# Kernel optimization log

Measured on AMD Instinct MI355X. Metric: run time of the kernel, lower is better.

Reference implementation:

```python
import jax, jax.numpy as jnp
import numpy as np
from jax import lax

B, N, C_IN, C_OUT = 4, 8192, 64, 128
STRIDE, RADIUS, K, L = 4, 0.1, 32, 2
EPS = 1e-5
M = N // STRIDE


def _bn(x, g, b):
    # training-mode batch norm, channel-first layout (B, C, ...)
    axes = (0,) + tuple(range(2, x.ndim))
    mean = jnp.mean(x, axis=axes, keepdims=True)
    var = jnp.mean((x - mean) ** 2, axis=axes, keepdims=True)
    sh = (1, -1) + (1,) * (x.ndim - 2)
    return (x - mean) * lax.rsqrt(var + EPS) * g.reshape(sh) + b.reshape(sh)


def _fps(points, m):
    # farthest point sampling starting at index 0 (matches fps_cuda semantics)
    b, n, _ = points.shape
    bi = jnp.arange(b)

    def body(carry, _):
        dis, last = carry
        lp = points[bi, last]  # (b,3)
        d = jnp.sum((points - lp[:, None, :]) ** 2, -1)
        dis = jnp.minimum(dis, d)
        return (dis, jnp.argmax(dis, -1).astype(jnp.int32)), last

    init = (jnp.full((b, n), 1e10, points.dtype), jnp.zeros((b,), jnp.int32))
    _, idx = lax.scan(body, init, None, length=m)
    return idx.T  # (b, m)


def _ball_query(radius, k, centroids, points, features):
    # first k points within radius of each centroid; pad with first hit
    b, n, _ = points.shape
    d2 = jnp.sum((centroids[:, :, None, :] - points[:, None, :, :]) ** 2, -1)  # (b,m,n)
    key = jnp.where(d2 < radius * radius, jnp.arange(n, dtype=jnp.int32), n)
    neg, _ = lax.top_k(-key, k)  # k smallest keys = first k in-ball indices
    sel = -neg  # (b,m,k)
    sel = jnp.where(sel == n, sel[..., :1], sel)
    sel = jnp.clip(sel, 0, n - 1)
    bi = jnp.arange(b)[:, None, None]
    gp = jnp.transpose(points[bi, sel], (0, 3, 2, 1))  # (b,3,k,m)
    gf = None
    if features is not None:
        gf = jnp.transpose(features[bi, sel], (0, 3, 2, 1))  # (b,c,k,m)
    return gp, gf


def _forward(pos, x, p):
    b, n, _ = pos.shape
    m = n // STRIDE
    bi = jnp.arange(b)[:, None]
    fps_idx = _fps(pos, m)
    centroids = pos[bi, fps_idx]  # (b,m,3)
    # x_mlp: 1x1 conv + BN + ReLU
    f = jax.nn.relu(_bn(jnp.einsum('bnc,oc->bon', x, p['W_x']), p['g_x'], p['b_x']))
    feats = jnp.transpose(f, (0, 2, 1))  # (b,n,C_OUT)
    gp, gf = _ball_query(RADIUS, K, centroids, pos, feats)
    cT = jnp.transpose(centroids, (0, 2, 1))[:, :, None, :]  # (b,3,1,m)
    gp = (gp - cT) / RADIUS
    gp = jax.nn.relu(_bn(jnp.einsum('bckm,oc->bokm', gp, p['W_ps']), p['g_ps'], p['b_ps']))
    xf = jnp.transpose(jnp.max(gf + gp, axis=2), (0, 2, 1))  # (b,m,C_OUT)
    # gen_pe on downsampled points
    R2 = RADIUS * 2
    gpe, _ = _ball_query(R2, K, centroids, centroids, None)
    gpe = (gpe - cT) / R2
    pe = jax.nn.relu(_bn(jnp.einsum('bckm,oc->bokm', gpe, p['W_pe']), p['g_pe'], p['b_pe']))
    # InvResMLP blocks
    for i in range(L):
        xc = jnp.transpose(xf, (0, 2, 1))  # (b,C,m)
        xc = jax.nn.relu(_bn(jnp.einsum('bcm,oc->bom', xc, p['W1'][i]), p['g1'][i], p['b1'][i]))
        feats_i = jnp.transpose(xc, (0, 2, 1))  # (b,m,C)
        _, gfi = _ball_query(R2, K, centroids, centroids, feats_i)
        g = jnp.max(gfi + pe, axis=2)  # (b,C,m)
        g = jax.nn.relu(_bn(jnp.einsum('bcm,oc->bom', g, p['W2a'][i]), p['g2a'][i], p['b2a'][i]))
        g = _bn(jnp.einsum('bcm,oc->bom', g, p['W2b'][i]), p['g2b'][i], p['b2b'][i])
        xf = jax.nn.relu(feats_i + jnp.transpose(g, (0, 2, 1)))
    return centroids, xf


def setup_inputs() -> dict:
    key = jax.random.key(0)
    ks = jax.random.split(key, 12)
    d = {
        'pos': jax.random.uniform(ks[0], (B, N, 3), jnp.float32),
        'x': jax.random.normal(ks[1], (B, N, C_IN), jnp.float32),
        'W_x': jax.random.normal(ks[2], (C_OUT, C_IN), jnp.float32) * 0.05,
        'g_x': jnp.ones((C_OUT,), jnp.float32), 'b_x': jnp.zeros((C_OUT,), jnp.float32),
        'W_ps': jax.random.normal(ks[3], (C_OUT, 3), jnp.float32) * 0.1,
        'g_ps': jnp.ones((C_OUT,), jnp.float32), 'b_ps': jnp.zeros((C_OUT,), jnp.float32),
        'W_pe': jax.random.normal(ks[4], (C_OUT, 3), jnp.float32) * 0.1,
        'g_pe': jnp.ones((C_OUT,), jnp.float32), 'b_pe': jnp.zeros((C_OUT,), jnp.float32),
        'W1': jax.random.normal(ks[5], (L, C_OUT, C_OUT), jnp.float32) * 0.05,
        'g1': jnp.ones((L, C_OUT), jnp.float32), 'b1': jnp.zeros((L, C_OUT), jnp.float32),
        'W2a': jax.random.normal(ks[6], (L, C_OUT, C_OUT), jnp.float32) * 0.05,
        'g2a': jnp.ones((L, C_OUT), jnp.float32), 'b2a': jnp.zeros((L, C_OUT), jnp.float32),
        'W2b': jax.random.normal(ks[7], (L, C_OUT, C_OUT), jnp.float32) * 0.05,
        'g2b': jnp.ones((L, C_OUT), jnp.float32), 'b2b': jnp.zeros((L, C_OUT), jnp.float32),
    }
    return d


def reference(pos, x, W_x, g_x, b_x, W_ps, g_ps, b_ps, W_pe, g_pe, b_pe,
              W1, g1, b1, W2a, g2a, b2a, W2b, g2b, b2b):
    p = dict(W_x=W_x, g_x=g_x, b_x=b_x, W_ps=W_ps, g_ps=g_ps, b_ps=b_ps,
             W_pe=W_pe, g_pe=g_pe, b_pe=b_pe, W1=W1, g1=g1, b1=b1,
             W2a=W2a, g2a=g2a, b2a=b2a, W2b=W2b, g2b=g2b, b2b=b2b)
    return _forward(pos, x, p)
```

## Files before the change

### kernel.cpp

```cpp
#include <hip/hip_runtime.h>


#define BB 4
#define NN 8192
#define MM 2048
#define HM 1024
#define KK 32
#define CI 64
#define CO 128
#define SG 16
#define CAPH 192

typedef float vf2 __attribute__((ext_vector_type(2)));

#define ST_X 0
#define MO_PS 256
#define MO_PE 272
#define ST1 288
#define ST2A (288 + 2 * SG * 256)
#define ST2B (ST2A + 2 * SG * 256)
#define ST_TOTAL (ST2B + 512)

__device__ __forceinline__ float sq3(float dx, float dy, float dz) {
#pragma clang fp contract(off)
  return dx * dx + dy * dy + dz * dz;
}

__device__ __forceinline__ void fin_stats_d(const double* st, float gam,
                                            float bet, double cnt, int ch,
                                            float* sc, float* sh) {
  double mean = st[ch] / cnt;
  double var = st[128 + ch] / cnt - mean * mean;
  if (var < 0) var = 0;
  double s = (double)gam / sqrt(var + 1e-5);
  *sc = (float)s;
  *sh = (float)((double)bet - mean * s);
}

__device__ __forceinline__ void fin_grp_d(const double* st, float gam,
                                          float bet, double cnt, int ch,
                                          float* sc, float* sh) {
  double sum = 0, ssq = 0;
#pragma unroll
  for (int g = 0; g < SG; g++) {
    sum += st[g * 256 + ch];
    ssq += st[g * 256 + 128 + ch];
  }
  double mean = sum / cnt;
  double var = ssq / cnt - mean * mean;
  if (var < 0) var = 0;
  double s = (double)gam / sqrt(var + 1e-5);
  *sc = (float)s;
  *sh = (float)((double)bet - mean * s);
}

__device__ __forceinline__ void fin_mom_d(const double* mo, const float* Wrow,
                                          float gam, float bet, double cnt,
                                          float* sc, float* sh) {
  double w0 = Wrow[0], w1 = Wrow[1], w2 = Wrow[2];
  double mx = mo[0] / cnt, my = mo[1] / cnt, mz = mo[2] / cnt;
  double sxx = mo[3] / cnt, sxy = mo[4] / cnt, sxz = mo[5] / cnt;
  double syy = mo[6] / cnt, syz = mo[7] / cnt, szz = mo[8] / cnt;
  double mean = w0 * mx + w1 * my + w2 * mz;
  double ey2 = w0 * w0 * sxx + w1 * w1 * syy + w2 * w2 * szz +
               2.0 * (w0 * w1 * sxy + w0 * w2 * sxz + w1 * w2 * syz);
  double var = ey2 - mean * mean;
  if (var < 0) var = 0;
  double s = (double)gam / sqrt(var + 1e-5);
  *sc = (float)s;
  *sh = (float)((double)bet - mean * s);
}

template <int CTRL>
__device__ __forceinline__ int dpp_i(int v) {
  return __builtin_amdgcn_update_dpp(v, v, CTRL, 0xF, 0xF, false);
}
template <int CTRL>
__device__ __forceinline__ float dpp_f(float v) {
  return __int_as_float(dpp_i<CTRL>(__float_as_int(v)));
}

#define FT 512
#define NP 8
#define NW 8

__device__ __forceinline__ void bq_grid(
    int pair, const float* __restrict__ pts, int npts,
    const float4* __restrict__ gxyz, const int* __restrict__ gstart, int G,
    float gs, float rad, float rsq, float inv_r, int* __restrict__ sel,
    const float* __restrict__ cent, int lane, int* __restrict__ s_hitw,
    int* __restrict__ s_selw, float* __restrict__ s_momw) {
  const float* C = cent + (size_t)pair * 3;
  float cx = C[0], cy = C[1], cz = C[2];
  unsigned long long ltm = (1ull << lane) - 1ull;
  int x0 = (int)((cx - rad - 1e-5f) * gs); x0 = x0 < 0 ? 0 : x0;
  int x1 = (int)((cx + rad + 1e-5f) * gs); x1 = x1 > G - 1 ? G - 1 : x1;
  int y0 = (int)((cy - rad - 1e-5f) * gs); y0 = y0 < 0 ? 0 : y0;
  int y1 = (int)((cy + rad + 1e-5f) * gs); y1 = y1 > G - 1 ? G - 1 : y1;
  int z0 = (int)((cz - rad - 1e-5f) * gs); z0 = z0 < 0 ? 0 : z0;
  int z1 = (int)((cz + rad + 1e-5f) * gs); z1 = z1 > G - 1 ? G - 1 : z1;
  int cnt = 0;
  for (int zz = z0; zz <= z1; zz++) {
    for (int yy = y0; yy <= y1; yy++) {
      int brow = (zz * G + yy) * G;
      int sbeg = gstart[brow + x0];
      int send = gstart[brow + x1 + 1];
      for (int base = sbeg; base < send; base += 64) {
        int j = base + lane;
        bool h = false;
        int pi = 0;
        if (j < send) {
          float4 v = gxyz[j];
          pi = __float_as_int(v.w);
          h = sq3(v.x - cx, v.y - cy, v.z - cz) < rsq;
        }
        unsigned long long mb = __ballot(h);
        if (mb) {
          int k = cnt + __popcll(mb & ltm);
          if (h && k < CAPH) s_hitw[k] = pi;
          cnt += __popcll(mb);
        }
      }
    }
  }
  __syncthreads();
  int total;
  if (cnt <= CAPH) {
    for (int l = lane; l < cnt; l += 64) {
      int v = s_hitw[l];
      int rk = 0;
      for (int j = 0; j < cnt; j++) rk += (s_hitw[j] < v);
      if (rk < KK) s_selw[rk] = v;
    }
    total = cnt < KK ? cnt : KK;
  } else {
    int bcnt = 0;
    int nit = npts >> 6;
    for (int ch = 0; ch < nit; ch++) {
      int i0 = (ch << 6) + lane;
      float a0 = pts[i0 * 3 + 0], a1 = pts[i0 * 3 + 1], a2 = pts[i0 * 3 + 2];
      bool h = sq3(a0 - cx, a1 - cy, a2 - cz) < rsq;
      unsigned long long mb = __ballot(h);
      if (mb) {
        int k = bcnt + __popcll(mb & ltm);
        if (h && k < KK) s_selw[k] = i0;
        bcnt += __popcll(mb);
      }
      if (bcnt >= KK) break;
    }
    total = bcnt < KK ? bcnt : KK;
  }
  __syncthreads();
  int myidx = 0;
  if (lane < KK) {
    int v = (lane < total) ? s_selw[lane] : s_selw[0];
    sel[(size_t)pair * KK + lane] = v;
    myidx = v;
  }
  float gx = 0.f, gy = 0.f, gz = 0.f;
  if (lane < KK) {
    gx = (pts[myidx * 3 + 0] - cx) * inv_r;
    gy = (pts[myidx * 3 + 1] - cy) * inv_r;
    gz = (pts[myidx * 3 + 2] - cz) * inv_r;
  }
  float v9[9] = {gx, gy, gz, gx * gx, gx * gy, gx * gz, gy * gy, gy * gz,
                 gz * gz};
#pragma unroll
  for (int j = 0; j < 9; j++) {
#pragma unroll
    for (int off = 32; off > 0; off >>= 1) v9[j] += __shfl_xor(v9[j], off);
  }
  if (lane == 0) {
#pragma unroll
    for (int j = 0; j < 9; j++) s_momw[j] = v9[j];
  }
}

__global__ __launch_bounds__(FT) void k_fps_conv(
    const float* __restrict__ pos, const float* __restrict__ x,
    const float* __restrict__ W_x, float* __restrict__ cent,
    float* __restrict__ fpre, double* __restrict__ stats,
    float* __restrict__ gds, int* __restrict__ pg_start,
    float4* __restrict__ pg_xyz) {
  __shared__ alignas(16) unsigned long long s_key[2][NW];
  __shared__ alignas(16) float s_pts[NN * 3];
  __shared__ alignas(16) float s_cent[MM * 3];
  int t = threadIdx.x;
  if (blockIdx.x >= BB + 256) {
    int bb = blockIdx.x - (BB + 256);
    const float* P = pos + (size_t)bb * NN * 3;
    int* cb = (int*)s_pts;
    int* rb = cb + 1024;
    for (int i = t; i < 1000; i += FT) cb[i] = 0;
    __syncthreads();
    for (int i = t; i < NN; i += FT) {
      float px = P[i * 3 + 0], py = P[i * 3 + 1], pz = P[i * 3 + 2];
      int bx = (int)(px * 10.f); bx = bx > 9 ? 9 : bx;
      int by = (int)(py * 10.f); by = by > 9 ? 9 : by;
      int bz = (int)(pz * 10.f); bz = bz > 9 ? 9 : bz;
      atomicAdd(&cb[(bz * 10 + by) * 10 + bx], 1);
    }
    __syncthreads();
    if (t == 0) {
      int acc = 0;
      for (int j = 0; j < 1000; j++) {
        pg_start[bb * 1024 + j] = acc;
        rb[j] = acc;
        acc += cb[j];
      }
      pg_start[bb * 1024 + 1000] = acc;
    }
    __syncthreads();
    for (int i = t; i < NN; i += FT) {
      float px = P[i * 3 + 0], py = P[i * 3 + 1], pz = P[i * 3 + 2];
      int bx = (int)(px * 10.f); bx = bx > 9 ? 9 : bx;
      int by = (int)(py * 10.f); by = by > 9 ? 9 : by;
      int bz = (int)(pz * 10.f); bz = bz > 9 ? 9 : bz;
      int slot = atomicAdd(&rb[(bz * 10 + by) * 10 + bx], 1);
      float4 v;
      v.x = px; v.y = py; v.z = pz; v.w = __int_as_float(i);
      pg_xyz[(size_t)bb * NN + slot] = v;
    }
    return;
  }
  if (blockIdx.x >= BB) {
    int cb2 = blockIdx.x - BB;
    int o = t & 127, q = t >> 7;
    float4 w[CI / 4];
    const float4* Wv = (const float4*)(W_x + (size_t)o * CI);
#pragma unroll
    for (int i = 0; i < CI / 4; i++) w[i] = Wv[i];
    int row0 = cb2 * 128;
    float ssum = 0.f, ssq = 0.f;
    for (int r = 0; r < 128; r += 4) {
      int row = __builtin_amdgcn_readfirstlane(row0 + r + q);
      const float* xr = x + (size_t)row * CI;
      float acc = 0.f;
#pragma unroll
      for (int i = 0; i < CI / 4; i++) {
        float4 a = *(const float4*)(xr + 4 * i);
        acc += a.x * w[i].x + a.y * w[i].y + a.z * w[i].z + a.w * w[i].w;
      }
      fpre[(size_t)row * CO + o] = acc;
      ssum += acc;
      ssq += acc * acc;
    }
    atomicAdd(&stats[ST_X + o], (double)ssum);
    atomicAdd(&stats[ST_X + 128 + o], (double)ssq);
    return;
  }
  int b = blockIdx.x;
  const float* P = pos + (size_t)b * NN * 3;
  float* C = cent + (size_t)b * MM * 3;
  int lane = t & 63, w = t >> 6;
  int ws = __builtin_amdgcn_readfirstlane(w);
  for (int i = t; i < (NN * 3) / 4; i += FT) {
    ((float4*)s_pts)[i] = ((const float4*)P)[i];
  }
  vf2 px[NP], py[NP], pz[NP], ds[NP];
#pragma unroll
  for (int s = 0; s < NP; s++) {
    int ia = (2 * s) * FT + t;
    int ib = ia + FT;
    px[s] = (vf2){P[ia * 3 + 0], P[ib * 3 + 0]};
    py[s] = (vf2){P[ia * 3 + 1], P[ib * 3 + 1]};
    pz[s] = (vf2){P[ia * 3 + 2], P[ib * 3 + 2]};
    ds[s] = (vf2){1e10f, 1e10f};
  }
  float lx = P[0], ly = P[1], lz = P[2];
  if (t == 0) {
    s_cent[0] = lx;
    s_cent[1] = ly;
    s_cent[2] = lz;
  }
  __syncthreads();
  for (int m = 1; m < HM; m++) {
    vf2 l2x = (vf2){lx, lx}, l2y = (vf2){ly, ly}, l2z = (vf2){lz, lz};
    vf2 bmax = (vf2){-1.0f, -1.0f};
    {
#pragma clang fp contract(off)
#pragma unroll
      for (int s = 0; s < NP; s++) {
        vf2 dx = px[s] - l2x;
        vf2 dy = py[s] - l2y;
        vf2 dz = pz[s] - l2z;
        vf2 d2 = dx * dx + dy * dy + dz * dz;
        vf2 nd = __builtin_elementwise_min(ds[s], d2);
        ds[s] = nd;
        bmax = __builtin_elementwise_max(bmax, nd);
      }
    }
    float bv = fmaxf(bmax.x, bmax.y);
    bv = fmaxf(bv, dpp_f<0x111>(bv));
    bv = fmaxf(bv, dpp_f<0x112>(bv));
    bv = fmaxf(bv, dpp_f<0x114>(bv));
    bv = fmaxf(bv, dpp_f<0x118>(bv));
    bv = fmaxf(bv, dpp_f<0x142>(bv));
    bv = fmaxf(bv, dpp_f<0x143>(bv));
    float wmax =
        __int_as_float(__builtin_amdgcn_readlane(__float_as_int(bv), 63));
    unsigned idxw = 0xffffffffu;
#pragma unroll
    for (int s = NP - 1; s >= 0; s--) {
      unsigned long long mby = __ballot(ds[s].y == wmax);
      unsigned basey = (unsigned)((2 * s) * FT + FT + (ws << 6));
      if (mby) idxw = basey + (unsigned)(__ffsll((long long)mby) - 1);
      unsigned long long mbx = __ballot(ds[s].x == wmax);
      unsigned basex = (unsigned)((2 * s) * FT + (ws << 6));
      if (mbx) idxw = basex + (unsigned)(__ffsll((long long)mbx) - 1);
    }
    int pb = m & 1;
    if (lane == 0) {
      s_key[pb][ws] = ((unsigned long long)__float_as_uint(wmax) << 32) |
                      (unsigned long long)(~idxw);
    }
    __syncthreads();
    const ulonglong2* kp = (const ulonglong2*)(&s_key[pb][0]);
    ulonglong2 q0 = kp[0];
    ulonglong2 q1 = kp[1];
    ulonglong2 q2 = kp[2];
    ulonglong2 q3 = kp[3];
    unsigned long long a0 = q0.x > q0.y ? q0.x : q0.y;
    unsigned long long a1 = q1.x > q1.y ? q1.x : q1.y;
    unsigned long long a2 = q2.x > q2.y ? q2.x : q2.y;
    unsigned long long a3 = q3.x > q3.y ? q3.x : q3.y;
    a0 = a0 > a1 ? a0 : a1;
    a2 = a2 > a3 ? a2 : a3;
    unsigned long long kw = a0 > a2 ? a0 : a2;
    unsigned gidx = ~(unsigned)(kw & 0xffffffffull);
    lx = s_pts[gidx * 3 + 0];
    ly = s_pts[gidx * 3 + 1];
    lz = s_pts[gidx * 3 + 2];
    if (t == 0) {
      s_cent[m * 3 + 0] = lx;
      s_cent[m * 3 + 1] = ly;
      s_cent[m * 3 + 2] = lz;
    }
  }
  __syncthreads();
  for (int i = t; i < (HM * 3) / 4; i += FT) {
    ((float4*)C)[i] = ((const float4*)s_cent)[i];
  }
  float2* gd = (float2*)gds + (size_t)b * NP * FT;
#pragma unroll
  for (int s = 0; s < NP; s++) {
    float2 v;
    v.x = ds[s].x;
    v.y = ds[s].y;
    gd[s * FT + t] = v;
  }
}

__global__ __launch_bounds__(FT) void k_fps_bq(
    const float* __restrict__ pos, float* __restrict__ cent,
    const float* __restrict__ gds, int* __restrict__ sel1,
    double* __restrict__ stats, const int* __restrict__ pg_start,
    const float4* __restrict__ pg_xyz) {
  __shared__ alignas(16) unsigned long long s_key[2][NW];
  __shared__ alignas(16) float s_pts[NN * 3];
  __shared__ alignas(16) float s_cent[MM * 3];
  __shared__ int s_hit[NW][CAPH];
  __shared__ int s_sel[NW][KK];
  __shared__ float s_mom[NW][9];
  int t = threadIdx.x;
  int lane = t & 63, w = t >> 6;
  if (blockIdx.x >= BB) {
    int pi = (blockIdx.x - BB) * 8 + w;
    int bb = pi >> 10, mi = pi & (HM - 1);
    int pair = bb * MM + mi;
    bq_grid(pair, pos + (size_t)bb * NN * 3, NN, pg_xyz + (size_t)bb * NN,
            pg_start + bb * 1024, 10, 10.f, 0.1f, 0.01f, 10.f, sel1, cent,
            lane, s_hit[w], s_sel[w], s_mom[w]);
    __syncthreads();
    if (t < 9) {
      double a = (double)s_mom[0][t];
#pragma unroll
      for (int j = 1; j < NW; j++) a += s_mom[j][t];
      atomicAdd(&stats[MO_PS + t], a);
    }
    return;
  }
  int b = blockIdx.x;
  const float* P = pos + (size_t)b * NN * 3;
  float* C = cent + (size_t)b * MM * 3;
  int ws = __builtin_amdgcn_readfirstlane(w);
  for (int i = t; i < (NN * 3) / 4; i += FT) {
    ((float4*)s_pts)[i] = ((const float4*)P)[i];
  }
  vf2 px[NP], py[NP], pz[NP], ds[NP];
  const float2* gd = (const float2*)gds + (size_t)b * NP * FT;
#pragma unroll
  for (int s = 0; s < NP; s++) {
    int ia = (2 * s) * FT + t;
    int ib = ia + FT;
    px[s] = (vf2){P[ia * 3 + 0], P[ib * 3 + 0]};
    py[s] = (vf2){P[ia * 3 + 1], P[ib * 3 + 1]};
    pz[s] = (vf2){P[ia * 3 + 2], P[ib * 3 + 2]};
    float2 v = gd[s * FT + t];
    ds[s] = (vf2){v.x, v.y};
  }
  float lx = C[(HM - 1) * 3 + 0];
  float ly = C[(HM - 1) * 3 + 1];
  float lz = C[(HM - 1) * 3 + 2];
  __syncthreads();
  for (int m = HM; m < MM; m++) {
    vf2 l2x = (vf2){lx, lx}, l2y = (vf2){ly, ly}, l2z = (vf2){lz, lz};
    vf2 bmax = (vf2){-1.0f, -1.0f};
    {
#pragma clang fp contract(off)
#pragma unroll
      for (int s = 0; s < NP; s++) {
        vf2 dx = px[s] - l2x;
        vf2 dy = py[s] - l2y;
        vf2 dz = pz[s] - l2z;
        vf2 d2 = dx * dx + dy * dy + dz * dz;
        vf2 nd = __builtin_elementwise_min(ds[s], d2);
        ds[s] = nd;
        bmax = __builtin_elementwise_max(bmax, nd);
      }
    }
    float bv = fmaxf(bmax.x, bmax.y);
    bv = fmaxf(bv, dpp_f<0x111>(bv));
    bv = fmaxf(bv, dpp_f<0x112>(bv));
    bv = fmaxf(bv, dpp_f<0x114>(bv));
    bv = fmaxf(bv, dpp_f<0x118>(bv));
    bv = fmaxf(bv, dpp_f<0x142>(bv));
    bv = fmaxf(bv, dpp_f<0x143>(bv));
    float wmax =
        __int_as_float(__builtin_amdgcn_readlane(__float_as_int(bv), 63));
    unsigned idxw = 0xffffffffu;
#pragma unroll
    for (int s = NP - 1; s >= 0; s--) {
      unsigned long long mby = __ballot(ds[s].y == wmax);
      unsigned basey = (unsigned)((2 * s) * FT + FT + (ws << 6));
      if (mby) idxw = basey + (unsigned)(__ffsll((long long)mby) - 1);
      unsigned long long mbx = __ballot(ds[s].x == wmax);
      unsigned basex = (unsigned)((2 * s) * FT + (ws << 6));
      if (mbx) idxw = basex + (unsigned)(__ffsll((long long)mbx) - 1);
    }
    int pb = m & 1;
    if (lane == 0) {
      s_key[pb][ws] = ((unsigned long long)__float_as_uint(wmax) << 32) |
                      (unsigned long long)(~idxw);
    }
    __syncthreads();
    const ulonglong2* kp = (const ulonglong2*)(&s_key[pb][0]);
    ulonglong2 q0 = kp[0];
    ulonglong2 q1 = kp[1];
    ulonglong2 q2 = kp[2];
    ulonglong2 q3 = kp[3];
    unsigned long long a0 = q0.x > q0.y ? q0.x : q0.y;
    unsigned long long a1 = q1.x > q1.y ? q1.x : q1.y;
    unsigned long long a2 = q2.x > q2.y ? q2.x : q2.y;
    unsigned long long a3 = q3.x > q3.y ? q3.x : q3.y;
    a0 = a0 > a1 ? a0 : a1;
    a2 = a2 > a3 ? a2 : a3;
    unsigned long long kw = a0 > a2 ? a0 : a2;
    unsigned gidx = ~(unsigned)(kw & 0xffffffffull);
    lx = s_pts[gidx * 3 + 0];
    ly = s_pts[gidx * 3 + 1];
    lz = s_pts[gidx * 3 + 2];
    if (t == 0) {
      s_cent[m * 3 + 0] = lx;
      s_cent[m * 3 + 1] = ly;
      s_cent[m * 3 + 2] = lz;
    }
  }
  __syncthreads();
  for (int i = t + (HM * 3) / 4; i < (MM * 3) / 4; i += FT) {
    ((float4*)C)[i] = ((const float4*)s_cent)[i];
  }
}

__global__ __launch_bounds__(256) void k_bin_cent(const float* __restrict__ cent,
                                                  int* __restrict__ cg_start,
                                                  float4* __restrict__ cg_xyz) {
  __shared__ int cb[128], rb[128];
  int t = threadIdx.x, bb = blockIdx.x;
  const float* C = cent + (size_t)bb * MM * 3;
  for (int i = t; i < 125; i += 256) cb[i] = 0;
  __syncthreads();
  for (int i = t; i < MM; i += 256) {
    float px = C[i * 3 + 0], py = C[i * 3 + 1], pz = C[i * 3 + 2];
    int bx = (int)(px * 5.f); bx = bx > 4 ? 4 : bx;
    int by = (int)(py * 5.f); by = by > 4 ? 4 : by;
    int bz = (int)(pz * 5.f); bz = bz > 4 ? 4 : bz;
    atomicAdd(&cb[(bz * 5 + by) * 5 + bx], 1);
  }
  __syncthreads();
  if (t == 0) {
    int acc = 0;
    for (int j = 0; j < 125; j++) {
      cg_start[bb * 128 + j] = acc;
      rb[j] = acc;
      acc += cb[j];
    }
    cg_start[bb * 128 + 125] = acc;
  }
  __syncthreads();
  for (int i = t; i < MM; i += 256) {
    float px = C[i * 3 + 0], py = C[i * 3 + 1], pz = C[i * 3 + 2];
    int bx = (int)(px * 5.f); bx = bx > 4 ? 4 : bx;
    int by = (int)(py * 5.f); by = by > 4 ? 4 : by;
    int bz = (int)(pz * 5.f); bz = bz > 4 ? 4 : bz;
    int slot = atomicAdd(&rb[(bz * 5 + by) * 5 + bx], 1);
    float4 v;
    v.x = px; v.y = py; v.z = pz; v.w = __int_as_float(i);
    cg_xyz[(size_t)bb * MM + slot] = v;
  }
}

__global__ __launch_bounds__(256) void k_bq_rest(
    const float* __restrict__ pos, const float* __restrict__ cent,
    const int* __restrict__ pg_start, const float4* __restrict__ pg_xyz,
    const int* __restrict__ cg_start, const float4* __restrict__ cg_xyz,
    int* __restrict__ sel1, int* __restrict__ sel2,
    double* __restrict__ stats) {
  __shared__ int s_hit[4][CAPH];
  __shared__ int s_sel[4][KK];
  __shared__ float s_mom[4][9];
  int t = threadIdx.x, lane = t & 63, w = t >> 6;
  int mo;
  if (blockIdx.x < (BB * (MM - HM)) / 4) {
    int pi = blockIdx.x * 4 + w;
    int bb = pi >> 10;
    int mi = (pi & (HM - 1)) + HM;
    int pair = bb * MM + mi;
    bq_grid(pair, pos + (size_t)bb * NN * 3, NN, pg_xyz + (size_t)bb * NN,
            pg_start + bb * 1024, 10, 10.f, 0.1f, 0.01f, 10.f, sel1, cent,
            lane, s_hit[w], s_sel[w], s_mom[w]);
    mo = MO_PS;
  } else {
    int pi = (blockIdx.x - (BB * (MM - HM)) / 4) * 4 + w;
    int bb = pi >> 11;
    bq_grid(pi, cent + (size_t)bb * MM * 3, MM, cg_xyz + (size_t)bb * MM,
            cg_start + bb * 128, 5, 5.f, 0.2f, 0.04f, 5.f, sel2, cent, lane,
            s_hit[w], s_sel[w], s_mom[w]);
    mo = MO_PE;
  }
  __syncthreads();
  if (t < 9) {
    double a = (double)s_mom[0][t] + s_mom[1][t] + s_mom[2][t] + s_mom[3][t];
    atomicAdd(&stats[mo + t], a);
  }
}

__global__ __launch_bounds__(128) void k_xf_conv1(
    const float* __restrict__ pos, const float* __restrict__ cent,
    const int* __restrict__ sel1, const float* __restrict__ fpre,
    const float* __restrict__ Wps, const float* __restrict__ g_ps,
    const float* __restrict__ b_ps, const float* __restrict__ g_x,
    const float* __restrict__ b_x, const double* __restrict__ stats,
    const float* __restrict__ W1, float* __restrict__ y1a,
    double* __restrict__ st1out) {
  int pair = blockIdx.x;
  int b = pair >> 11;
  int o = threadIdx.x;
  float sx, hx, sp, hp;
  fin_stats_d(stats + ST_X, g_x[o], b_x[o], (double)(BB * NN), o, &sx, &hx);
  fin_mom_d(stats + MO_PS, Wps + o * 3, g_ps[o], b_ps[o],
            (double)(BB * MM * KK), &sp, &hp);
  float w0 = Wps[o * 3 + 0], w1 = Wps[o * 3 + 1], w2 = Wps[o * 3 + 2];
  const float* C = cent + (size_t)pair * 3;
  float cx = C[0], cy = C[1], cz = C[2];
  const float* P = pos + (size_t)b * NN * 3;
  const float* F = fpre + (size_t)b * NN * CO;
  __shared__ int s_idx[KK];
  __shared__ float s_xf[128];
  if (o < KK) s_idx[o] = sel1[(size_t)pair * KK + o];
  __syncthreads();
  float acc = -1e30f;
#pragma unroll 4
  for (int k = 0; k < KK; k++) {
    int idx = __builtin_amdgcn_readfirstlane(s_idx[k]);
    float gx = (P[idx * 3 + 0] - cx) * 10.0f;
    float gy = (P[idx * 3 + 1] - cy) * 10.0f;
    float gz = (P[idx * 3 + 2] - cz) * 10.0f;
    float y = fmaxf((w0 * gx + w1 * gy + w2 * gz) * sp + hp, 0.f);
    float f = fmaxf(F[(size_t)idx * CO + o] * sx + hx, 0.f);
    float v = y + f;
    acc = v > acc ? v : acc;
  }
  s_xf[o] = acc;
  __syncthreads();
  const float4* Wv = (const float4*)(W1 + (size_t)o * CO);
  const float4* gv = (const float4*)s_xf;
  float dot = 0.f;
#pragma unroll
  for (int i = 0; i < CO / 4; i++) {
    float4 a = gv[i];
    float4 ww = Wv[i];
    dot += a.x * ww.x + a.y * ww.y + a.z * ww.z + a.w * ww.w;
  }
  y1a[(size_t)pair * CO + o] = dot;
  int grp = pair & (SG - 1);
  atomicAdd(&st1out[grp * 256 + o], (double)dot);
  atomicAdd(&st1out[grp * 256 + 128 + o], (double)(dot * dot));
}

__global__ __launch_bounds__(256) void k_conv_bnin(
    const float* __restrict__ in, const float* __restrict__ W,
    const double* __restrict__ st_grp, const float* __restrict__ gam,
    const float* __restrict__ bet, float* __restrict__ out,
    double* __restrict__ stats, int rows_per_block) {
  __shared__ float s_sc[128], s_sh[128];
  int t = threadIdx.x;
  if (t < 128) {
    fin_grp_d(st_grp, gam[t], bet[t], (double)(BB * MM), t, &s_sc[t],
              &s_sh[t]);
  }
  __syncthreads();
  int o = t & 127, half = t >> 7;
  float4 w[CO / 4];
  const float4* Wv = (const float4*)(W + (size_t)o * CO);
#pragma unroll
  for (int i = 0; i < CO / 4; i++) w[i] = Wv[i];
  int row0 = blockIdx.x * rows_per_block;
  float ssum = 0.f, ssq = 0.f;
  for (int r = 0; r < rows_per_block; r += 2) {
    int row = __builtin_amdgcn_readfirstlane(row0 + r + half);
    const float* xr = in + (size_t)row * CO;
    float acc = 0.f;
#pragma unroll
    for (int i = 0; i < CO / 4; i++) {
      float4 a = *(const float4*)(xr + 4 * i);
      a.x = fmaxf(a.x * s_sc[4 * i + 0] + s_sh[4 * i + 0], 0.f);
      a.y = fmaxf(a.y * s_sc[4 * i + 1] + s_sh[4 * i + 1], 0.f);
      a.z = fmaxf(a.z * s_sc[4 * i + 2] + s_sh[4 * i + 2], 0.f);
      a.w = fmaxf(a.w * s_sc[4 * i + 3] + s_sh[4 * i + 3], 0.f);
      acc += a.x * w[i].x + a.y * w[i].y + a.z * w[i].z + a.w * w[i].w;
    }
    out[(size_t)row * CO + o] = acc;
    ssum += acc;
    ssq += acc * acc;
  }
  atomicAdd(&stats[o], (double)ssum);
  atomicAdd(&stats[128 + o], (double)ssq);
}

__global__ __launch_bounds__(256) void k_conv_resid(
    const float* __restrict__ y1prev, const float* __restrict__ y2bprev,
    const double* __restrict__ st1p, const float* __restrict__ g1p,
    const float* __restrict__ b1p, const double* __restrict__ st2bp,
    const float* __restrict__ g2bp, const float* __restrict__ b2bp,
    const float* __restrict__ W, float* __restrict__ y1out,
    double* __restrict__ stats, int rows_per_block) {
  __shared__ float s_s1[128], s_h1[128], s_s2[128], s_h2[128];
  int t = threadIdx.x;
  if (t < 128) {
    fin_grp_d(st1p, g1p[t], b1p[t], (double)(BB * MM), t, &s_s1[t], &s_h1[t]);
    fin_stats_d(st2bp, g2bp[t], b2bp[t], (double)(BB * MM), t, &s_s2[t],
                &s_h2[t]);
  }
  __syncthreads();
  int o = t & 127, half = t >> 7;
  float4 w[CO / 4];
  const float4* Wv = (const float4*)(W + (size_t)o * CO);
#pragma unroll
  for (int i = 0; i < CO / 4; i++) w[i] = Wv[i];
  int row0 = blockIdx.x * rows_per_block;
  float ssum = 0.f, ssq = 0.f;
  for (int r = 0; r < rows_per_block; r += 2) {
    int row = __builtin_amdgcn_readfirstlane(row0 + r + half);
    const float* ar = y1prev + (size_t)row * CO;
    const float* br = y2bprev + (size_t)row * CO;
    float acc = 0.f;
#pragma unroll
    for (int i = 0; i < CO / 4; i++) {
      float4 a = *(const float4*)(ar + 4 * i);
      float4 bb = *(const float4*)(br + 4 * i);
      float x0 = fmaxf(fmaxf(a.x * s_s1[4 * i + 0] + s_h1[4 * i + 0], 0.f) +
                           (bb.x * s_s2[4 * i + 0] + s_h2[4 * i + 0]), 0.f);
      float x1 = fmaxf(fmaxf(a.y * s_s1[4 * i + 1] + s_h1[4 * i + 1], 0.f) +
                           (bb.y * s_s2[4 * i + 1] + s_h2[4 * i + 1]), 0.f);
      float x2 = fmaxf(fmaxf(a.z * s_s1[4 * i + 2] + s_h1[4 * i + 2], 0.f) +
                           (bb.z * s_s2[4 * i + 2] + s_h2[4 * i + 2]), 0.f);
      float x3 = fmaxf(fmaxf(a.w * s_s1[4 * i + 3] + s_h1[4 * i + 3], 0.f) +
                           (bb.w * s_s2[4 * i + 3] + s_h2[4 * i + 3]), 0.f);
      acc += x0 * w[i].x + x1 * w[i].y + x2 * w[i].z + x3 * w[i].w;
    }
    y1out[(size_t)row * CO + o] = acc;
    ssum += acc;
    ssq += acc * acc;
  }
  int grp = blockIdx.x & (SG - 1);
  atomicAdd(&stats[grp * 256 + o], (double)ssum);
  atomicAdd(&stats[grp * 256 + 128 + o], (double)ssq);
}

__global__ __launch_bounds__(128) void k_gconv(
    const float* __restrict__ cent, const int* __restrict__ sel2,
    const float* __restrict__ y1in, const double* __restrict__ st1,
    const float* __restrict__ g1v, const float* __restrict__ b1v,
    const double* __restrict__ mo_pe, const float* __restrict__ Wpe,
    const float* __restrict__ gpe, const float* __restrict__ bpe,
    const float* __restrict__ W2a, float* __restrict__ y2a,
    double* __restrict__ st2a) {
  int pair = blockIdx.x;
  int b = pair >> 11;
  int o = threadIdx.x;
  float s1, h1, se, he;
  fin_grp_d(st1, g1v[o], b1v[o], (double)(BB * MM), o, &s1, &h1);
  fin_mom_d(mo_pe, Wpe + o * 3, gpe[o], bpe[o], (double)(BB * MM * KK), &se,
            &he);
  float w0 = Wpe[o * 3 + 0], w1 = Wpe[o * 3 + 1], w2 = Wpe[o * 3 + 2];
  const float* C = cent + (size_t)pair * 3;
  float cx = C[0], cy = C[1], cz = C[2];
  const float* CB = cent + (size_t)b * MM * 3;
  const float* Y = y1in + (size_t)b * MM * CO;
  __shared__ int s_idx[KK];
  __shared__ float s_g[128];
  if (o < KK) s_idx[o] = sel2[(size_t)pair * KK + o];
  __syncthreads();
  float acc = -1e30f;
#pragma unroll 4
  for (int k = 0; k < KK; k++) {
    int idx = __builtin_amdgcn_readfirstlane(s_idx[k]);
    float gx = (CB[idx * 3 + 0] - cx) * 5.0f;
    float gy = (CB[idx * 3 + 1] - cy) * 5.0f;
    float gz = (CB[idx * 3 + 2] - cz) * 5.0f;
    float pe = fmaxf((w0 * gx + w1 * gy + w2 * gz) * se + he, 0.f);
    float f = fmaxf(Y[(size_t)idx * CO + o] * s1 + h1, 0.f);
    float v = pe + f;
    acc = v > acc ? v : acc;
  }
  s_g[o] = acc;
  __syncthreads();
  const float4* Wv = (const float4*)(W2a + (size_t)o * CO);
  const float4* gv = (const float4*)s_g;
  float dot = 0.f;
#pragma unroll
  for (int i = 0; i < CO / 4; i++) {
    float4 a = gv[i];
    float4 ww = Wv[i];
    dot += a.x * ww.x + a.y * ww.y + a.z * ww.z + a.w * ww.w;
  }
  y2a[(size_t)pair * CO + o] = dot;
  int grp = pair & (SG - 1);
  atomicAdd(&st2a[grp * 256 + o], (double)dot);
  atomicAdd(&st2a[grp * 256 + 128 + o], (double)(dot * dot));
}

__global__ __launch_bounds__(256) void k_resid_fin(
    const float* __restrict__ y1b, const double* __restrict__ st1,
    const float* __restrict__ g1v, const float* __restrict__ b1v,
    const float* __restrict__ y2b, const double* __restrict__ st2b,
    const float* __restrict__ g2bv, const float* __restrict__ b2bv,
    float* __restrict__ xf) {
  int i = blockIdx.x * 256 + threadIdx.x;
  int o = i & 127;
  float s1, h1, s2, h2;
  fin_grp_d(st1, g1v[o], b1v[o], (double)(BB * MM), o, &s1, &h1);
  fin_stats_d(st2b, g2bv[o], b2bv[o], (double)(BB * MM), o, &s2, &h2);
  float f = fmaxf(y1b[i] * s1 + h1, 0.f);
  float v = y2b[i] * s2 + h2;
  xf[i] = fmaxf(f + v, 0.f);
}

extern "C" void kernel_launch(void* const* d_in, const int* in_sizes, int n_in,
                              void* d_out, int out_size, void* d_ws,
                              size_t ws_size, hipStream_t stream) {
  const float* pos = (const float*)d_in[0];
  const float* x = (const float*)d_in[1];
  const float* W_x = (const float*)d_in[2];
  const float* g_x = (const float*)d_in[3];
  const float* b_x = (const float*)d_in[4];
  const float* W_ps = (const float*)d_in[5];
  const float* g_ps = (const float*)d_in[6];
  const float* b_ps = (const float*)d_in[7];
  const float* W_pe = (const float*)d_in[8];
  const float* g_pe = (const float*)d_in[9];
  const float* b_pe = (const float*)d_in[10];
  const float* W1 = (const float*)d_in[11];
  const float* g1 = (const float*)d_in[12];
  const float* b1 = (const float*)d_in[13];
  const float* W2a = (const float*)d_in[14];
  const float* g2a = (const float*)d_in[15];
  const float* b2a = (const float*)d_in[16];
  const float* W2b = (const float*)d_in[17];
  const float* g2b = (const float*)d_in[18];
  const float* b2b = (const float*)d_in[19];

  float* cent = (float*)d_out;
  float* xf = cent + (size_t)BB * MM * 3;

  char* p = (char*)d_ws;
  double* stats = (double*)p; p += (size_t)ST_TOTAL * sizeof(double);
  int* sel1 = (int*)p;        p += (size_t)BB * MM * KK * sizeof(int);
  int* sel2 = (int*)p;        p += (size_t)BB * MM * KK * sizeof(int);
  float* fpre = (float*)p;    p += (size_t)BB * NN * CO * sizeof(float);
  float* y1a = (float*)p;     p += (size_t)BB * MM * CO * sizeof(float);
  float* y1b = (float*)p;     p += (size_t)BB * MM * CO * sizeof(float);
  float* y2a = (float*)p;     p += (size_t)BB * MM * CO * sizeof(float);
  float* y2b = (float*)p;     p += (size_t)BB * MM * CO * sizeof(float);
  float* gds = (float*)p;     p += (size_t)BB * NP * FT * 2 * sizeof(float);
  float4* pg_xyz = (float4*)p; p += (size_t)BB * NN * sizeof(float4);
  float4* cg_xyz = (float4*)p; p += (size_t)BB * MM * sizeof(float4);
  int* pg_start = (int*)p;    p += (size_t)BB * 1024 * sizeof(int);
  int* cg_start = (int*)p;    p += (size_t)BB * 128 * sizeof(int);

  hipMemsetAsync(stats, 0, (size_t)ST_TOTAL * sizeof(double), stream);
  k_fps_conv<<<BB + 256 + BB, FT, 0, stream>>>(pos, x, W_x, cent, fpre, stats,
                                               gds, pg_start, pg_xyz);
  k_fps_bq<<<BB + (BB * HM) / 8, FT, 0, stream>>>(pos, cent, gds, sel1, stats,
                                                  pg_start, pg_xyz);
  k_bin_cent<<<BB, 256, 0, stream>>>(cent, cg_start, cg_xyz);
  k_bq_rest<<<(BB * (MM - HM)) / 4 + (BB * MM) / 4, 256, 0, stream>>>(
      pos, cent, pg_start, pg_xyz, cg_start, cg_xyz, sel1, sel2, stats);
  k_xf_conv1<<<BB * MM, 128, 0, stream>>>(pos, cent, sel1, fpre, W_ps, g_ps,
                                          b_ps, g_x, b_x, stats, W1, y1a,
                                          stats + ST1);
  k_gconv<<<BB * MM, 128, 0, stream>>>(cent, sel2, y1a, stats + ST1, g1, b1,
                                       stats + MO_PE, W_pe, g_pe, b_pe, W2a,
                                       y2a, stats + ST2A);
  k_conv_bnin<<<128, 256, 0, stream>>>(y2a, W2b, stats + ST2A, g2a, b2a, y2b,
                                       stats + ST2B, 64);
  k_conv_resid<<<128, 256, 0, stream>>>(
      y1a, y2b, stats + ST1, g1, b1, stats + ST2B, g2b, b2b, W1 + CO * CO, y1b,
      stats + ST1 + SG * 256, 64);
  k_gconv<<<BB * MM, 128, 0, stream>>>(cent, sel2, y1b, stats + ST1 + SG * 256,
                                       g1 + 128, b1 + 128, stats + MO_PE, W_pe,
                                       g_pe, b_pe, W2a + CO * CO, y2a,
                                       stats + ST2A + SG * 256);
  k_conv_bnin<<<128, 256, 0, stream>>>(y2a, W2b + CO * CO,
                                       stats + ST2A + SG * 256, g2a + 128,
                                       b2a + 128, y2b, stats + ST2B + 256, 64);
  k_resid_fin<<<(BB * MM * CO) / 256, 256, 0, stream>>>(
      y1b, stats + ST1 + SG * 256, g1 + 128, b1 + 128, y2b,
      stats + ST2B + 256, g2b + 128, b2b + 128, xf);
}
```

Before: 2.547 ms.

## Batch 32 pairs per block in gather-conv kernels and pre-reduce BN stats

k_xf_conv1 and k_gconv now launch 256 blocks of 512 threads instead of 8192 blocks of 128. Each block processes 32 centroid pairs as 4 sub-groups over 8 iterations. BN scale/shift finalization and the Wps/Wpe weight loads happen once per block into shared memory instead of once per pair. Per-channel sum and sum-of-squares are accumulated in registers and reduced in shared memory, so each block issues 256 double atomics instead of 256 per pair. The cost is fewer resident waves per CU for a latency-bound gather loop, plus extra barriers inside the pair loop.

```diff
diff --git a/kernel.cpp b/kernel.cpp
--- a/kernel.cpp
+++ b/kernel.cpp
@@ -545,7 +545,7 @@
   }
 }
 
-__global__ __launch_bounds__(128) void k_xf_conv1(
+__global__ __launch_bounds__(512) void k_xf_conv1(
     const float* __restrict__ pos, const float* __restrict__ cent,
     const int* __restrict__ sel1, const float* __restrict__ fpre,
     const float* __restrict__ Wps, const float* __restrict__ g_ps,
@@ -553,49 +553,78 @@
     const float* __restrict__ b_x, const double* __restrict__ stats,
     const float* __restrict__ W1, float* __restrict__ y1a,
     double* __restrict__ st1out) {
-  int pair = blockIdx.x;
-  int b = pair >> 11;
-  int o = threadIdx.x;
-  float sx, hx, sp, hp;
-  fin_stats_d(stats + ST_X, g_x[o], b_x[o], (double)(BB * NN), o, &sx, &hx);
-  fin_mom_d(stats + MO_PS, Wps + o * 3, g_ps[o], b_ps[o],
-            (double)(BB * MM * KK), &sp, &hp);
-  float w0 = Wps[o * 3 + 0], w1 = Wps[o * 3 + 1], w2 = Wps[o * 3 + 2];
-  const float* C = cent + (size_t)pair * 3;
-  float cx = C[0], cy = C[1], cz = C[2];
-  const float* P = pos + (size_t)b * NN * 3;
-  const float* F = fpre + (size_t)b * NN * CO;
-  __shared__ int s_idx[KK];
-  __shared__ float s_xf[128];
-  if (o < KK) s_idx[o] = sel1[(size_t)pair * KK + o];
-  __syncthreads();
-  float acc = -1e30f;
+  __shared__ alignas(16) float s_sx[128], s_hx[128], s_sp[128], s_hp[128];
+  __shared__ alignas(16) float s_w0[128], s_w1[128], s_w2[128];
+  __shared__ alignas(16) int s_idx[4][KK];
+  __shared__ alignas(16) float s_xf[4][128];
+  __shared__ alignas(16) double s_rs[4][128], s_rq[4][128];
+  int t = threadIdx.x, bid = blockIdx.x;
+  if (t < 128) {
+    float sx, hx, sp, hp;
+    fin_stats_d(stats + ST_X, g_x[t], b_x[t], (double)(BB * NN), t, &sx, &hx);
+    fin_mom_d(stats + MO_PS, Wps + t * 3, g_ps[t], b_ps[t],
+              (double)(BB * MM * KK), &sp, &hp);
+    s_sx[t] = sx;
+    s_hx[t] = hx;
+    s_sp[t] = sp;
+    s_hp[t] = hp;
+    s_w0[t] = Wps[t * 3 + 0];
+    s_w1[t] = Wps[t * 3 + 1];
+    s_w2[t] = Wps[t * 3 + 2];
+  }
+  __syncthreads();
+  int o = t & 127, sub = t >> 7;
+  float sx = s_sx[o], hx = s_hx[o], sp = s_sp[o], hp = s_hp[o];
+  float w0 = s_w0[o], w1 = s_w1[o], w2 = s_w2[o];
+  double rsum = 0.0, rsq = 0.0;
+  for (int p = 0; p < 8; p++) {
+    int pair = bid * 32 + p * 4 + sub;
+    int b = pair >> 11;
+    const float* C = cent + (size_t)pair * 3;
+    float cx = C[0], cy = C[1], cz = C[2];
+    const float* P = pos + (size_t)b * NN * 3;
+    const float* F = fpre + (size_t)b * NN * CO;
+    if (o < KK) s_idx[sub][o] = sel1[(size_t)pair * KK + o];
+    __syncthreads();
+    float acc = -1e30f;
 #pragma unroll 4
-  for (int k = 0; k < KK; k++) {
-    int idx = __builtin_amdgcn_readfirstlane(s_idx[k]);
-    float gx = (P[idx * 3 + 0] - cx) * 10.0f;
-    float gy = (P[idx * 3 + 1] - cy) * 10.0f;
-    float gz = (P[idx * 3 + 2] - cz) * 10.0f;
-    float y = fmaxf((w0 * gx + w1 * gy + w2 * gz) * sp + hp, 0.f);
-    float f = fmaxf(F[(size_t)idx * CO + o] * sx + hx, 0.f);
-    float v = y + f;
-    acc = v > acc ? v : acc;
-  }
-  s_xf[o] = acc;
-  __syncthreads();
-  const float4* Wv = (const float4*)(W1 + (size_t)o * CO);
-  const float4* gv = (const float4*)s_xf;
-  float dot = 0.f;
-#pragma unroll
-  for (int i = 0; i < CO / 4; i++) {
-    float4 a = gv[i];
-    float4 ww = Wv[i];
-    dot += a.x * ww.x + a.y * ww.y + a.z * ww.z + a.w * ww.w;
-  }
-  y1a[(size_t)pair * CO + o] = dot;
-  int grp = pair & (SG - 1);
-  atomicAdd(&st1out[grp * 256 + o], (double)dot);
-  atomicAdd(&st1out[grp * 256 + 128 + o], (double)(dot * dot));
+    for (int k = 0; k < KK; k++) {
+      int idx = __builtin_amdgcn_readfirstlane(s_idx[sub][k]);
+      float gx = (P[idx * 3 + 0] - cx) * 10.0f;
+      float gy = (P[idx * 3 + 1] - cy) * 10.0f;
+      float gz = (P[idx * 3 + 2] - cz) * 10.0f;
+      float y = fmaxf((w0 * gx + w1 * gy + w2 * gz) * sp + hp, 0.f);
+      float f = fmaxf(F[(size_t)idx * CO + o] * sx + hx, 0.f);
+      float v = y + f;
+      acc = v > acc ? v : acc;
+    }
+    s_xf[sub][o] = acc;
+    __syncthreads();
+    const float4* Wv = (const float4*)(W1 + (size_t)o * CO);
+    const float4* gv = (const float4*)(&s_xf[sub][0]);
+    float dot = 0.f;
+#pragma unroll
+    for (int i = 0; i < CO / 4; i++) {
+      float4 a = gv[i];
+      float4 ww = Wv[i];
+      dot += a.x * ww.x + a.y * ww.y + a.z * ww.z + a.w * ww.w;
+    }
+    y1a[(size_t)pair * CO + o] = dot;
+    rsum += (double)dot;
+    rsq += (double)(dot * dot);
+  }
+  s_rs[sub][o] = rsum;
+  s_rq[sub][o] = rsq;
+  __syncthreads();
+  int grp = bid & (SG - 1);
+  if (t < 128) {
+    double a = s_rs[0][t] + s_rs[1][t] + s_rs[2][t] + s_rs[3][t];
+    atomicAdd(&st1out[grp * 256 + t], a);
+  } else if (t < 256) {
+    int c = t - 128;
+    double a = s_rq[0][c] + s_rq[1][c] + s_rq[2][c] + s_rq[3][c];
+    atomicAdd(&st1out[grp * 256 + 128 + c], a);
+  }
 }
 
 __global__ __launch_bounds__(256) void k_conv_bnin(
@@ -688,7 +717,7 @@
   atomicAdd(&stats[grp * 256 + 128 + o], (double)ssq);
 }
 
-__global__ __launch_bounds__(128) void k_gconv(
+__global__ __launch_bounds__(512) void k_gconv(
     const float* __restrict__ cent, const int* __restrict__ sel2,
     const float* __restrict__ y1in, const double* __restrict__ st1,
     const float* __restrict__ g1v, const float* __restrict__ b1v,
@@ -696,49 +725,78 @@
     const float* __restrict__ gpe, const float* __restrict__ bpe,
     const float* __restrict__ W2a, float* __restrict__ y2a,
     double* __restrict__ st2a) {
-  int pair = blockIdx.x;
-  int b = pair >> 11;
-  int o = threadIdx.x;
-  float s1, h1, se, he;
-  fin_grp_d(st1, g1v[o], b1v[o], (double)(BB * MM), o, &s1, &h1);
-  fin_mom_d(mo_pe, Wpe + o * 3, gpe[o], bpe[o], (double)(BB * MM * KK), &se,
-            &he);
-  float w0 = Wpe[o * 3 + 0], w1 = Wpe[o * 3 + 1], w2 = Wpe[o * 3 + 2];
-  const float* C = cent + (size_t)pair * 3;
-  float cx = C[0], cy = C[1], cz = C[2];
-  const float* CB = cent + (size_t)b * MM * 3;
-  const float* Y = y1in + (size_t)b * MM * CO;
-  __shared__ int s_idx[KK];
-  __shared__ float s_g[128];
-  if (o < KK) s_idx[o] = sel2[(size_t)pair * KK + o];
-  __syncthreads();
-  float acc = -1e30f;
+  __shared__ alignas(16) float s_s1[128], s_h1[128], s_se[128], s_he[128];
+  __shared__ alignas(16) float s_w0[128], s_w1[128], s_w2[128];
+  __shared__ alignas(16) int s_idx[4][KK];
+  __shared__ alignas(16) float s_g[4][128];
+  __shared__ alignas(16) double s_rs[4][128], s_rq[4][128];
+  int t = threadIdx.x, bid = blockIdx.x;
+  if (t < 128) {
+    float s1, h1, se, he;
+    fin_grp_d(st1, g1v[t], b1v[t], (double)(BB * MM), t, &s1, &h1);
+    fin_mom_d(mo_pe, Wpe + t * 3, gpe[t], bpe[t], (double)(BB * MM * KK), &se,
+              &he);
+    s_s1[t] = s1;
+    s_h1[t] = h1;
+    s_se[t] = se;
+    s_he[t] = he;
+    s_w0[t] = Wpe[t * 3 + 0];
+    s_w1[t] = Wpe[t * 3 + 1];
+    s_w2[t] = Wpe[t * 3 + 2];
+  }
+  __syncthreads();
+  int o = t & 127, sub = t >> 7;
+  float s1 = s_s1[o], h1 = s_h1[o], se = s_se[o], he = s_he[o];
+  float w0 = s_w0[o], w1 = s_w1[o], w2 = s_w2[o];
+  double rsum = 0.0, rsq = 0.0;
+  for (int p = 0; p < 8; p++) {
+    int pair = bid * 32 + p * 4 + sub;
+    int b = pair >> 11;
+    const float* C = cent + (size_t)pair * 3;
+    float cx = C[0], cy = C[1], cz = C[2];
+    const float* CB = cent + (size_t)b * MM * 3;
+    const float* Y = y1in + (size_t)b * MM * CO;
+    if (o < KK) s_idx[sub][o] = sel2[(size_t)pair * KK + o];
+    __syncthreads();
+    float acc = -1e30f;
 #pragma unroll 4
-  for (int k = 0; k < KK; k++) {
-    int idx = __builtin_amdgcn_readfirstlane(s_idx[k]);
-    float gx = (CB[idx * 3 + 0] - cx) * 5.0f;
-    float gy = (CB[idx * 3 + 1] - cy) * 5.0f;
-    float gz = (CB[idx * 3 + 2] - cz) * 5.0f;
-    float pe = fmaxf((w0 * gx + w1 * gy + w2 * gz) * se + he, 0.f);
-    float f = fmaxf(Y[(size_t)idx * CO + o] * s1 + h1, 0.f);
-    float v = pe + f;
-    acc = v > acc ? v : acc;
-  }
-  s_g[o] = acc;
-  __syncthreads();
-  const float4* Wv = (const float4*)(W2a + (size_t)o * CO);
-  const float4* gv = (const float4*)s_g;
-  float dot = 0.f;
-#pragma unroll
-  for (int i = 0; i < CO / 4; i++) {
-    float4 a = gv[i];
-    float4 ww = Wv[i];
-    dot += a.x * ww.x + a.y * ww.y + a.z * ww.z + a.w * ww.w;
-  }
-  y2a[(size_t)pair * CO + o] = dot;
-  int grp = pair & (SG - 1);
-  atomicAdd(&st2a[grp * 256 + o], (double)dot);
-  atomicAdd(&st2a[grp * 256 + 128 + o], (double)(dot * dot));
+    for (int k = 0; k < KK; k++) {
+      int idx = __builtin_amdgcn_readfirstlane(s_idx[sub][k]);
+      float gx = (CB[idx * 3 + 0] - cx) * 5.0f;
+      float gy = (CB[idx * 3 + 1] - cy) * 5.0f;
+      float gz = (CB[idx * 3 + 2] - cz) * 5.0f;
+      float pe = fmaxf((w0 * gx + w1 * gy + w2 * gz) * se + he, 0.f);
+      float f = fmaxf(Y[(size_t)idx * CO + o] * s1 + h1, 0.f);
+      float v = pe + f;
+      acc = v > acc ? v : acc;
+    }
+    s_g[sub][o] = acc;
+    __syncthreads();
+    const float4* Wv = (const float4*)(W2a + (size_t)o * CO);
+    const float4* gv = (const float4*)(&s_g[sub][0]);
+    float dot = 0.f;
+#pragma unroll
+    for (int i = 0; i < CO / 4; i++) {
+      float4 a = gv[i];
+      float4 ww = Wv[i];
+      dot += a.x * ww.x + a.y * ww.y + a.z * ww.z + a.w * ww.w;
+    }
+    y2a[(size_t)pair * CO + o] = dot;
+    rsum += (double)dot;
+    rsq += (double)(dot * dot);
+  }
+  s_rs[sub][o] = rsum;
+  s_rq[sub][o] = rsq;
+  __syncthreads();
+  int grp = bid & (SG - 1);
+  if (t < 128) {
+    double a = s_rs[0][t] + s_rs[1][t] + s_rs[2][t] + s_rs[3][t];
+    atomicAdd(&st2a[grp * 256 + t], a);
+  } else if (t < 256) {
+    int c = t - 128;
+    double a = s_rq[0][c] + s_rq[1][c] + s_rq[2][c] + s_rq[3][c];
+    atomicAdd(&st2a[grp * 256 + 128 + c], a);
+  }
 }
 
 __global__ __launch_bounds__(256) void k_resid_fin(
@@ -807,21 +865,21 @@
   k_bin_cent<<<BB, 256, 0, stream>>>(cent, cg_start, cg_xyz);
   k_bq_rest<<<(BB * (MM - HM)) / 4 + (BB * MM) / 4, 256, 0, stream>>>(
       pos, cent, pg_start, pg_xyz, cg_start, cg_xyz, sel1, sel2, stats);
-  k_xf_conv1<<<BB * MM, 128, 0, stream>>>(pos, cent, sel1, fpre, W_ps, g_ps,
-                                          b_ps, g_x, b_x, stats, W1, y1a,
-                                          stats + ST1);
-  k_gconv<<<BB * MM, 128, 0, stream>>>(cent, sel2, y1a, stats + ST1, g1, b1,
-                                       stats + MO_PE, W_pe, g_pe, b_pe, W2a,
-                                       y2a, stats + ST2A);
+  k_xf_conv1<<<256, 512, 0, stream>>>(pos, cent, sel1, fpre, W_ps, g_ps,
+                                      b_ps, g_x, b_x, stats, W1, y1a,
+                                      stats + ST1);
+  k_gconv<<<256, 512, 0, stream>>>(cent, sel2, y1a, stats + ST1, g1, b1,
+                                   stats + MO_PE, W_pe, g_pe, b_pe, W2a, y2a,
+                                   stats + ST2A);
   k_conv_bnin<<<128, 256, 0, stream>>>(y2a, W2b, stats + ST2A, g2a, b2a, y2b,
                                        stats + ST2B, 64);
   k_conv_resid<<<128, 256, 0, stream>>>(
       y1a, y2b, stats + ST1, g1, b1, stats + ST2B, g2b, b2b, W1 + CO * CO, y1b,
       stats + ST1 + SG * 256, 64);
-  k_gconv<<<BB * MM, 128, 0, stream>>>(cent, sel2, y1b, stats + ST1 + SG * 256,
-                                       g1 + 128, b1 + 128, stats + MO_PE, W_pe,
-                                       g_pe, b_pe, W2a + CO * CO, y2a,
-                                       stats + ST2A + SG * 256);
+  k_gconv<<<256, 512, 0, stream>>>(cent, sel2, y1b, stats + ST1 + SG * 256,
+                                   g1 + 128, b1 + 128, stats + MO_PE, W_pe,
+                                   g_pe, b_pe, W2a + CO * CO, y2a,
+                                   stats + ST2A + SG * 256);
   k_conv_bnin<<<128, 256, 0, stream>>>(y2a, W2b + CO * CO,
                                        stats + ST2A + SG * 256, g2a + 128,
                                        b2a + 128, y2b, stats + ST2B + 256, 64);
```

Result: faster. 2.464 ms (median of 2 runs) (-3.2%).
